# Kernel tuning notes

Measured on AMD Instinct MI355X. Metric: run time of the kernel, lower is better.

The kernel has to match this reference:

```python
import jax, jax.numpy as jnp
import numpy as np
import math

B = 2048; H = 16; KL = 16; KR = 16; D = 64
K_MAX = 32; MAX_DEPTH = 12; DE = 32; DEPTH = 3


def setup_inputs() -> dict:
    key = jax.random.key(0)
    ks = jax.random.split(key, 8)
    def n(k, shape, s=1.0):
        return jax.random.normal(k, shape, dtype=jnp.float32) * s
    return {
        'f_left': n(ks[0], (B, H, KL, D)),
        'f_right': n(ks[1], (B, H, KR, D)),
        'gate_left_w': n(ks[2], (2 * D + DE, D), 0.02),
        'gate_left_b': jnp.full((D,), 0.5, jnp.float32),
        'gate_right_w': n(ks[3], (2 * D + DE, D), 0.02),
        'gate_right_b': jnp.full((D,), 0.5, jnp.float32),
        'parent_query_base': n(ks[4], (K_MAX, D), 0.02),
        'query_offset_w': n(ks[5], (DE, K_MAX * D), 0.02),
        'query_offset_b': jnp.zeros((K_MAX * D,), jnp.float32),
        'ln_gamma': jnp.ones((D,), jnp.float32),
        'ln_beta': jnp.zeros((D,), jnp.float32),
        'skip_proj_w': n(ks[6], (D, D), 0.02),
        'skip_alpha': jnp.float32(0.1),
        'wave_freq': jnp.linspace(0.3, 4.0, H, dtype=jnp.float32),
        'wave_damp': jnp.linspace(-3.0, 0.5, H, dtype=jnp.float32),
        'wave_phase': jnp.linspace(0.0, math.pi, H, dtype=jnp.float32),
        'depth': DEPTH,
    }


def _depth_vec(depth):
    # sinusoidal embedding row for `depth` (interleaved sin/cos)
    inv = jnp.exp(jnp.arange(0, DE, 2, dtype=jnp.float32) * (-math.log(10000.0) / DE))
    return jnp.stack([jnp.sin(depth * inv), jnp.cos(depth * inv)], axis=1).reshape(-1)


def _forward(f_left, f_right, glw, glb, grw, grb, pqb, qow, qob, g, b, spw, sa, wf, wd, wp, depth):
    # wave rotation of right child (complex multiply on split halves)
    scale = float(max(2 ** (MAX_DEPTH - depth), 1))
    alpha_d = jax.nn.softplus(wd) / scale
    omega_d = wf / scale
    phi_d = wp + depth * (math.pi / 4.0)
    decay = jnp.exp(-alpha_d * scale)
    pr = (decay * jnp.cos(omega_d * scale + phi_d))[None, :, None, None]  # (1,H,1,1)
    pi_ = (decay * jnp.sin(omega_d * scale + phi_d))[None, :, None, None]
    d2 = D // 2
    fr, fi = f_right[..., :d2], f_right[..., d2:]
    rot = jnp.concatenate([pr * fr - pi_ * fi, pi_ * fr + pr * fi], axis=-1)  # (B,H,KR,D)

    # depth-conditioned gating
    left_mean = f_left.mean(axis=2)   # (B,H,D)
    right_mean = rot.mean(axis=2)
    dv = _depth_vec(depth)            # (DE,)
    dvb = jnp.broadcast_to(dv, (f_left.shape[0], H, DE))
    gate_in = jnp.concatenate([left_mean, right_mean, dvb], axis=-1)  # (B,H,2D+DE)
    g_l = jax.nn.sigmoid(gate_in @ glw + glb)[:, :, None, :]
    g_r = jax.nn.sigmoid(gate_in @ grw + grb)[:, :, None, :]
    bank = jnp.concatenate([f_left * g_l, rot * g_r], axis=2)  # (B,H,KL+KR,D)

    # small-K attention with depth-offset parent queries
    k_parent = min(KL + KR, K_MAX)
    q_off = (dv @ qow + qob).reshape(K_MAX, D)
    pq = pqb[:k_parent] + q_off[:k_parent]  # (k_parent,D)
    attn = jax.nn.softmax(jnp.einsum('qd,bhkd->bhqk', pq, bank) / math.sqrt(D), axis=-1)
    parent_raw = jnp.einsum('bhqk,bhkd->bhqd', attn, bank)  # (B,H,k_parent,D)

    # layernorm over D (eps=1e-5, biased var as in torch)
    mu = parent_raw.mean(axis=-1, keepdims=True)
    var = parent_raw.var(axis=-1, keepdims=True)
    parent_norm = (parent_raw - mu) / jnp.sqrt(var + 1e-5) * g + b

    # gated skip from left mean
    skip = (left_mean @ spw)[:, :, None, :]
    return parent_norm + jax.nn.sigmoid(sa) * skip


def reference(f_left, f_right, gate_left_w, gate_left_b, gate_right_w, gate_right_b, parent_query_base, query_offset_w, query_offset_b, ln_gamma, ln_beta, skip_proj_w, skip_alpha, wave_freq, wave_damp, wave_phase, depth):
    return _forward(f_left, f_right, gate_left_w, gate_left_b, gate_right_w, gate_right_b, parent_query_base, query_offset_w, query_offset_b, ln_gamma, ln_beta, skip_proj_w, skip_alpha, wave_freq, wave_damp, wave_phase, depth)
```

## Files before the change

kernel.cpp:

```cpp
#include <hip/hip_runtime.h>
#include <math.h>

#define B_ 2048
#define H_ 16
#define D_ 64
#define DE_ 32
#define NK_ 32
#define KP_ 32

#define OFF_WTL 2048
#define OFF_WTR 10240
#define OFF_SPT 18432
#define OFF_BL  22528
#define WS_TOTAL 22656

typedef __attribute__((ext_vector_type(8)))  short short8;
typedef __attribute__((ext_vector_type(16))) float f32x16;
typedef __attribute__((ext_vector_type(4)))  unsigned int uint4v;

#define MFMA32(A,Bo,C) __builtin_amdgcn_mfma_f32_32x32x16_bf16(A,Bo,C,0,0,0)

__device__ __forceinline__ unsigned short bf16_rne(float x){
    unsigned u = __float_as_uint(x);
    unsigned r = u + 0x7fffu + ((u>>16)&1u);
    return (unsigned short)(r>>16);
}
__device__ __forceinline__ float bf16_to_f(unsigned short h){
    return __uint_as_float((unsigned)h << 16);
}
__device__ __forceinline__ unsigned pack2(unsigned short a, unsigned short b){
    return (unsigned)a | ((unsigned)b << 16);
}

__global__ void precompute(const float* __restrict__ pqb,
                           const float* __restrict__ qow,
                           const float* __restrict__ qob,
                           const float* __restrict__ glw,
                           const float* __restrict__ glb,
                           const float* __restrict__ grw,
                           const float* __restrict__ grb,
                           const float* __restrict__ spw,
                           const int*   __restrict__ depth_p,
                           float* __restrict__ ws)
{
    __shared__ float dvS[DE_];
    const int t = threadIdx.x;
    const int depth = depth_p[0];
    if (t < DE_) {
        int pi_ = t >> 1;
        float inv = expf(-(float)(2*pi_) * (logf(10000.f)/(float)DE_));
        float x = (float)depth * inv;
        dvS[t] = (t & 1) ? cosf(x) : sinf(x);
    }
    __syncthreads();
    int idx = blockIdx.x*256 + t;
    if (idx < 2048) {
        int q = idx >> 6, d = idx & 63;
        float acc = pqb[idx] + qob[idx];
        for (int i = 0; i < DE_; ++i) acc += dvS[i]*qow[i*2048 + idx];
        unsigned short hi = bf16_rne(acc);
        unsigned short lo = bf16_rne(acc - bf16_to_f(hi));
        int ds = d >> 4, h2 = (d>>3)&1, jj = d&7;
        int e = (ds*64 + (h2*32 + q))*8 + jj;
        unsigned short* wsu = (unsigned short*)ws;
        wsu[e]        = hi;
        wsu[2048 + e] = lo;
    } else if (idx < 2048 + 8192) {
        int j = idx - 2048; int d = j >> 7, i = j & 127;
        ws[OFF_WTL + j] = glw[i*64 + d];
    } else if (idx < 2048 + 16384) {
        int j = idx - (2048+8192); int d = j >> 7, i = j & 127;
        ws[OFF_WTR + j] = grw[i*64 + d];
    } else if (idx < 2048 + 16384 + 4096) {
        int j = idx - (2048+16384); int d = j >> 6, i = j & 63;
        ws[OFF_SPT + j] = spw[i*64 + d];
    } else if (idx < WS_TOTAL) {
        int j = idx - OFF_BL; int side = j >> 6, d = j & 63;
        const float* W = side ? grw : glw;
        float acc = side ? grb[d] : glb[d];
        for (int i = 0; i < DE_; ++i) acc += dvS[i]*W[(128+i)*64 + d];
        ws[OFF_BL + j] = acc;
    }
}

__global__ __launch_bounds__(256, 4)
void gwm_main(const float* __restrict__ fL, const float* __restrict__ fR,
              const float* __restrict__ lng, const float* __restrict__ lnb,
              const float* __restrict__ sa,
              const float* __restrict__ wf, const float* __restrict__ wd,
              const float* __restrict__ wp, const int* __restrict__ depth_p,
              const float* __restrict__ ws, float* __restrict__ out)
{
    __shared__ __align__(16) unsigned short bankH16[NK_*64];
    __shared__ __align__(16) unsigned short bankL16[NK_*64];
    __shared__ __align__(16) unsigned short bTH16[64*40];
    __shared__ __align__(16) unsigned short bTL16[64*40];
    __shared__ __align__(16) float partialS[8][64];
    __shared__ __align__(16) float lrS[128];
    __shared__ __align__(16) float glS[64], grS[64], addS[64], gamS[64];

    const int t    = threadIdx.x;
    const int pair = blockIdx.x;
    const int h    = pair & (H_-1);
    const int wv   = t >> 6;
    const int lane = t & 63;
    const int depth = depth_p[0];

    float wdv = wd[h];
    float sp = logf(1.f + expf(wdv));
    float decay = expf(-sp);
    float ang = wf[h] + wp[h] + (float)depth * 0.78539816339744831f;
    float pr  = decay * cosf(ang);
    float pim = decay * sinf(ang);

    const int kk = t >> 4;
    const int c  = t & 15;

    const size_t base = (size_t)pair * (16*64);
    float4 v4 = *(const float4*)(fL + base + kk*64 + 4*c);
    const float* fp = fR + base + kk*64;
    float2 fr2 = *(const float2*)(fp + 2*c);
    float2 fi2 = *(const float2*)(fp + 2*c + 32);
    float ro0 = pr*fr2.x - pim*fi2.x;
    float ro1 = pr*fr2.y - pim*fi2.y;
    float ro2 = pim*fr2.x + pr*fi2.x;
    float ro3 = pim*fr2.y + pr*fi2.y;

    float s0=v4.x, s1=v4.y, s2=v4.z, s3=v4.w;
    float u0=ro0, u1=ro1, u2=ro2, u3=ro3;
#define RED2(x) { x += __shfl_xor(x,16); x += __shfl_xor(x,32); }
    RED2(s0) RED2(s1) RED2(s2) RED2(s3)
    RED2(u0) RED2(u1) RED2(u2) RED2(u3)
    if (lane < 16) {
        *(float4*)(&partialS[wv][4*c])      = make_float4(s0,s1,s2,s3);
        *(float2*)(&partialS[4+wv][2*c])    = make_float2(u0,u1);
        *(float2*)(&partialS[4+wv][2*c+32]) = make_float2(u2,u3);
    }
    __syncthreads();

    if (t < 128) {
        int d = t & 63, side = t >> 6;
        const float* p = &partialS[side*4][0];
        lrS[t] = (p[d] + p[64+d] + p[128+d] + p[192+d]) * 0.0625f;
    }
    __syncthreads();

    if (wv < 2) {
        const float* Wt = ws + (wv ? OFF_WTR : OFF_WTL) + lane*128;
        float acc = ws[OFF_BL + wv*64 + lane];
        #pragma unroll 8
        for (int i = 0; i < 128; i += 4) {
            float4 w = *(const float4*)(Wt + i);
            float4 v = *(const float4*)(lrS + i);
            acc += w.x*v.x + w.y*v.y + w.z*v.z + w.w*v.w;
        }
        float g = 1.f / (1.f + __expf(-acc));
        (wv ? grS : glS)[lane] = g;
    } else if (wv == 2) {
        const float* Sp = ws + OFF_SPT + lane*64;
        float acc = 0.f;
        #pragma unroll 8
        for (int i = 0; i < 64; i += 4) {
            float4 w = *(const float4*)(Sp + i);
            float4 v = *(const float4*)(lrS + i);
            acc += w.x*v.x + w.y*v.y + w.z*v.z + w.w*v.w;
        }
        float ss = 1.f / (1.f + __expf(-sa[0]));
        addS[lane] = lnb[lane] + ss * acc;
    } else {
        gamS[lane] = lng[lane];
    }
    __syncthreads();

    const int hw = pair & 3;
    short8 qh0, qh1, qh2, qh3, ql0, ql1, ql2, ql3;
    if (wv == hw) {
        const unsigned short* wsu = (const unsigned short*)ws;
        qh0 = *(const short8*)(wsu + (0*64 + lane)*8);
        qh1 = *(const short8*)(wsu + (1*64 + lane)*8);
        qh2 = *(const short8*)(wsu + (2*64 + lane)*8);
        qh3 = *(const short8*)(wsu + (3*64 + lane)*8);
        ql0 = *(const short8*)(wsu + 2048 + (0*64 + lane)*8);
        ql1 = *(const short8*)(wsu + 2048 + (1*64 + lane)*8);
        ql2 = *(const short8*)(wsu + 2048 + (2*64 + lane)*8);
        ql3 = *(const short8*)(wsu + 2048 + (3*64 + lane)*8);
    }

    {
        float4 g4 = *(const float4*)(glS + 4*c);
        float b0 = v4.x*g4.x, b1 = v4.y*g4.y, b2 = v4.z*g4.z, b3 = v4.w*g4.w;
        unsigned short H0=bf16_rne(b0), H1=bf16_rne(b1), H2=bf16_rne(b2), H3=bf16_rne(b3);
        unsigned short L0=bf16_rne(b0-bf16_to_f(H0)), L1=bf16_rne(b1-bf16_to_f(H1));
        unsigned short L2=bf16_rne(b2-bf16_to_f(H2)), L3=bf16_rne(b3-bf16_to_f(H3));
        const int m = (kk & 7) << 3;
        int eo = kk*64 + ((4*c) ^ m);
        *(uint2*)(bankH16 + eo) = make_uint2(pack2(H0,H1), pack2(H2,H3));
        *(uint2*)(bankL16 + eo) = make_uint2(pack2(L0,L1), pack2(L2,L3));
        bTH16[(4*c+0)*40 + kk] = H0; bTH16[(4*c+1)*40 + kk] = H1;
        bTH16[(4*c+2)*40 + kk] = H2; bTH16[(4*c+3)*40 + kk] = H3;
        bTL16[(4*c+0)*40 + kk] = L0; bTL16[(4*c+1)*40 + kk] = L1;
        bTL16[(4*c+2)*40 + kk] = L2; bTL16[(4*c+3)*40 + kk] = L3;

        float2 ga = *(const float2*)(grS + 2*c);
        float2 gb = *(const float2*)(grS + 2*c + 32);
        float w0 = ro0*ga.x, w1 = ro1*ga.y, w2 = ro2*gb.x, w3 = ro3*gb.y;
        unsigned short R0=bf16_rne(w0), R1=bf16_rne(w1), R2=bf16_rne(w2), R3=bf16_rne(w3);
        unsigned short S0_=bf16_rne(w0-bf16_to_f(R0)), S1_=bf16_rne(w1-bf16_to_f(R1));
        unsigned short S2_=bf16_rne(w2-bf16_to_f(R2)), S3_=bf16_rne(w3-bf16_to_f(R3));
        const int row = (16+kk)*64;
        *(unsigned*)(bankH16 + row + ((2*c)    ^ m)) = pack2(R0,R1);
        *(unsigned*)(bankH16 + row + ((2*c+32) ^ m)) = pack2(R2,R3);
        *(unsigned*)(bankL16 + row + ((2*c)    ^ m)) = pack2(S0_,S1_);
        *(unsigned*)(bankL16 + row + ((2*c+32) ^ m)) = pack2(S2_,S3_);
        bTH16[(2*c  )*40 + 16+kk] = R0; bTH16[(2*c+1 )*40 + 16+kk] = R1;
        bTH16[(2*c+32)*40 + 16+kk] = R2; bTH16[(2*c+33)*40 + 16+kk] = R3;
        bTL16[(2*c  )*40 + 16+kk] = S0_; bTL16[(2*c+1 )*40 + 16+kk] = S1_;
        bTL16[(2*c+32)*40 + 16+kk] = S2_; bTL16[(2*c+33)*40 + 16+kk] = S3_;
    }
    __syncthreads();

    if (wv == hw) {
        const int q  = lane & 31;
        const int hh = lane >> 5;

        f32x16 A1, A2;
        #pragma unroll
        for (int i = 0; i < 16; ++i) { A1[i] = 0.f; A2[i] = 0.f; }
        const int sw = (q & 7) << 3;
        {
            int eo = q*64 + ((0*16 + hh*8) ^ sw);
            short8 ah = *(const short8*)(bankH16 + eo);
            short8 al = *(const short8*)(bankL16 + eo);
            A1 = MFMA32(ah, qh0, A1); A2 = MFMA32(ah, ql0, A2); A1 = MFMA32(al, qh0, A1);
        }
        {
            int eo = q*64 + ((1*16 + hh*8) ^ sw);
            short8 ah = *(const short8*)(bankH16 + eo);
            short8 al = *(const short8*)(bankL16 + eo);
            A1 = MFMA32(ah, qh1, A1); A2 = MFMA32(ah, ql1, A2); A1 = MFMA32(al, qh1, A1);
        }
        {
            int eo = q*64 + ((2*16 + hh*8) ^ sw);
            short8 ah = *(const short8*)(bankH16 + eo);
            short8 al = *(const short8*)(bankL16 + eo);
            A1 = MFMA32(ah, qh2, A1); A2 = MFMA32(ah, ql2, A2); A1 = MFMA32(al, qh2, A1);
        }
        {
            int eo = q*64 + ((3*16 + hh*8) ^ sw);
            short8 ah = *(const short8*)(bankH16 + eo);
            short8 al = *(const short8*)(bankL16 + eo);
            A1 = MFMA32(ah, qh3, A1); A2 = MFMA32(ah, ql3, A2); A1 = MFMA32(al, qh3, A1);
        }
        float sc[16];
        #pragma unroll
        for (int i = 0; i < 16; ++i) sc[i] = (A1[i] + A2[i]) * 0.125f;
        float mx = sc[0];
        #pragma unroll
        for (int i = 1; i < 16; ++i) mx = fmaxf(mx, sc[i]);
        mx = fmaxf(mx, __shfl_xor(mx, 32));
        float ssum = 0.f;
        #pragma unroll
        for (int i = 0; i < 16; ++i) { sc[i] = __expf(sc[i] - mx); ssum += sc[i]; }
        ssum += __shfl_xor(ssum, 32);
        float inv = 1.f / ssum;
        unsigned ch[8], cl[8], dh[8], dl[8];
        #pragma unroll
        for (int w = 0; w < 8; ++w) {
            float a0 = sc[2*w]*inv, a1 = sc[2*w+1]*inv;
            unsigned short Ha = bf16_rne(a0), Hb = bf16_rne(a1);
            unsigned short La = bf16_rne(a0 - bf16_to_f(Ha));
            unsigned short Lb = bf16_rne(a1 - bf16_to_f(Hb));
            ch[w] = pack2(Ha,Hb); cl[w] = pack2(La,Lb);
        }
        #pragma unroll
        for (int w = 0; w < 8; ++w) { dh[w] = __shfl_xor(ch[w],32); dl[w] = __shfl_xor(cl[w],32); }
        short8 Bh0, Bh1, Bl0, Bl1;
        if (hh == 0) {
            uint4v vh0 = {ch[0],ch[1],dh[0],dh[1]}, vl0 = {cl[0],cl[1],dl[0],dl[1]};
            uint4v vh1 = {ch[4],ch[5],dh[4],dh[5]}, vl1 = {cl[4],cl[5],dl[4],dl[5]};
            Bh0 = __builtin_bit_cast(short8, vh0); Bl0 = __builtin_bit_cast(short8, vl0);
            Bh1 = __builtin_bit_cast(short8, vh1); Bl1 = __builtin_bit_cast(short8, vl1);
        } else {
            uint4v vh0 = {dh[2],dh[3],ch[2],ch[3]}, vl0 = {dl[2],dl[3],cl[2],cl[3]};
            uint4v vh1 = {dh[6],dh[7],ch[6],ch[7]}, vl1 = {dl[6],dl[7],cl[6],cl[7]};
            Bh0 = __builtin_bit_cast(short8, vh0); Bl0 = __builtin_bit_cast(short8, vl0);
            Bh1 = __builtin_bit_cast(short8, vh1); Bl1 = __builtin_bit_cast(short8, vl1);
        }
        f32x16 P0, P1;
        {
            f32x16 p1, p2;
            #pragma unroll
            for (int i = 0; i < 16; ++i) { p1[i] = 0.f; p2[i] = 0.f; }
            int e0 = q*40 + hh*8;
            short8 Ah = *(const short8*)(bTH16 + e0);
            short8 Al = *(const short8*)(bTL16 + e0);
            p1 = MFMA32(Ah, Bh0, p1); p2 = MFMA32(Ah, Bl0, p2); p1 = MFMA32(Al, Bh0, p1);
            int e1 = q*40 + 16 + hh*8;
            Ah = *(const short8*)(bTH16 + e1);
            Al = *(const short8*)(bTL16 + e1);
            p1 = MFMA32(Ah, Bh1, p1); p2 = MFMA32(Ah, Bl1, p2); p1 = MFMA32(Al, Bh1, p1);
            P0 = p1 + p2;
        }
        {
            f32x16 p1, p2;
            #pragma unroll
            for (int i = 0; i < 16; ++i) { p1[i] = 0.f; p2[i] = 0.f; }
            int e0 = (32+q)*40 + hh*8;
            short8 Ah = *(const short8*)(bTH16 + e0);
            short8 Al = *(const short8*)(bTL16 + e0);
            p1 = MFMA32(Ah, Bh0, p1); p2 = MFMA32(Ah, Bl0, p2); p1 = MFMA32(Al, Bh0, p1);
            int e1 = (32+q)*40 + 16 + hh*8;
            Ah = *(const short8*)(bTH16 + e1);
            Al = *(const short8*)(bTL16 + e1);
            p1 = MFMA32(Ah, Bh1, p1); p2 = MFMA32(Ah, Bl1, p2); p1 = MFMA32(Al, Bh1, p1);
            P1 = p1 + p2;
        }
        float sum = 0.f;
        #pragma unroll
        for (int i = 0; i < 16; ++i) sum += P0[i] + P1[i];
        sum += __shfl_xor(sum, 32);
        float mu = sum * (1.f/64.f);
        float ssd = 0.f;
        #pragma unroll
        for (int i = 0; i < 16; ++i) {
            float d1 = P0[i]-mu, d2 = P1[i]-mu;
            ssd += d1*d1 + d2*d2;
        }
        ssd += __shfl_xor(ssd, 32);
        float rinv = 1.f / sqrtf(ssd*(1.f/64.f) + 1e-5f);
        float* outp = out + (size_t)pair*(KP_*D_) + (size_t)q*64;
        #pragma unroll
        for (int grp = 0; grp < 4; ++grp) {
            int d0 = grp*8 + hh*4;
            float4 gm = *(const float4*)(gamS + d0);
            float4 ad = *(const float4*)(addS + d0);
            float4 o;
            o.x = (P0[grp*4+0]-mu)*rinv*gm.x + ad.x;
            o.y = (P0[grp*4+1]-mu)*rinv*gm.y + ad.y;
            o.z = (P0[grp*4+2]-mu)*rinv*gm.z + ad.z;
            o.w = (P0[grp*4+3]-mu)*rinv*gm.w + ad.w;
            *(float4*)(outp + d0) = o;
            int d1 = 32 + d0;
            float4 gm1 = *(const float4*)(gamS + d1);
            float4 ad1 = *(const float4*)(addS + d1);
            float4 o1;
            o1.x = (P1[grp*4+0]-mu)*rinv*gm1.x + ad1.x;
            o1.y = (P1[grp*4+1]-mu)*rinv*gm1.y + ad1.y;
            o1.z = (P1[grp*4+2]-mu)*rinv*gm1.z + ad1.z;
            o1.w = (P1[grp*4+3]-mu)*rinv*gm1.w + ad1.w;
            *(float4*)(outp + d1) = o1;
        }
    }
}

extern "C" void kernel_launch(void* const* d_in, const int* in_sizes, int n_in,
                              void* d_out, int out_size, void* d_ws, size_t ws_size,
                              hipStream_t stream) {
    const float* fL  = (const float*)d_in[0];
    const float* fR  = (const float*)d_in[1];
    const float* glw = (const float*)d_in[2];
    const float* glb = (const float*)d_in[3];
    const float* grw = (const float*)d_in[4];
    const float* grb = (const float*)d_in[5];
    const float* pqb = (const float*)d_in[6];
    const float* qow = (const float*)d_in[7];
    const float* qob = (const float*)d_in[8];
    const float* lng = (const float*)d_in[9];
    const float* lnb = (const float*)d_in[10];
    const float* spw = (const float*)d_in[11];
    const float* sa  = (const float*)d_in[12];
    const float* wf  = (const float*)d_in[13];
    const float* wd  = (const float*)d_in[14];
    const float* wp  = (const float*)d_in[15];
    const int* depth = (const int*)d_in[16];
    float* ws  = (float*)d_ws;
    float* out = (float*)d_out;

    hipLaunchKernelGGL(precompute, dim3((WS_TOTAL+255)/256), dim3(256), 0, stream,
                       pqb, qow, qob, glw, glb, grw, grb, spw, depth, ws);
    hipLaunchKernelGGL(gwm_main, dim3(B_*H_), dim3(256), 0, stream,
                       fL, fR, lng, lnb, sa, wf, wd, wp, depth, ws, out);
}
```

Baseline: 712.3 us.

## Read gate weights in original layout with coalesced float4 loads; split MFMA accumulators

The precompute kernel no longer builds transposed copies of the gate and skip weights. The main kernel now reads them directly in row-major order: each 16-lane group handles one input row and four output columns with float4 loads, and shuffles reduce across the groups. This makes the per-block weight reads coalesced instead of strided per lane and shrinks the precompute work. Separately, the error-compensation MFMA chains now use independent accumulators, which shortens the dependent MFMA latency chains at the cost of extra registers.

```diff
diff --git a/kernel.cpp b/kernel.cpp
--- a/kernel.cpp
+++ b/kernel.cpp
@@ -8,11 +8,8 @@
 #define NK_ 32
 #define KP_ 32
 
-#define OFF_WTL 2048
-#define OFF_WTR 10240
-#define OFF_SPT 18432
-#define OFF_BL  22528
-#define WS_TOTAL 22656
+#define OFF_BL   2048
+#define WS_TOTAL 2176
 
 typedef __attribute__((ext_vector_type(8)))  short short8;
 typedef __attribute__((ext_vector_type(16))) float f32x16;
@@ -39,7 +36,6 @@
                            const float* __restrict__ glb,
                            const float* __restrict__ grw,
                            const float* __restrict__ grb,
-                           const float* __restrict__ spw,
                            const int*   __restrict__ depth_p,
                            float* __restrict__ ws)
 {
@@ -65,15 +61,6 @@
         unsigned short* wsu = (unsigned short*)ws;
         wsu[e]        = hi;
         wsu[2048 + e] = lo;
-    } else if (idx < 2048 + 8192) {
-        int j = idx - 2048; int d = j >> 7, i = j & 127;
-        ws[OFF_WTL + j] = glw[i*64 + d];
-    } else if (idx < 2048 + 16384) {
-        int j = idx - (2048+8192); int d = j >> 7, i = j & 127;
-        ws[OFF_WTR + j] = grw[i*64 + d];
-    } else if (idx < 2048 + 16384 + 4096) {
-        int j = idx - (2048+16384); int d = j >> 6, i = j & 63;
-        ws[OFF_SPT + j] = spw[i*64 + d];
     } else if (idx < WS_TOTAL) {
         int j = idx - OFF_BL; int side = j >> 6, d = j & 63;
         const float* W = side ? grw : glw;
@@ -85,6 +72,8 @@
 
 __global__ __launch_bounds__(256, 4)
 void gwm_main(const float* __restrict__ fL, const float* __restrict__ fR,
+              const float* __restrict__ glw, const float* __restrict__ grw,
+              const float* __restrict__ spw,
               const float* __restrict__ lng, const float* __restrict__ lnb,
               const float* __restrict__ sa,
               const float* __restrict__ wf, const float* __restrict__ wd,
@@ -145,30 +134,54 @@
     }
     __syncthreads();
 
-    if (wv < 2) {
-        const float* Wt = ws + (wv ? OFF_WTR : OFF_WTL) + lane*128;
-        float acc = ws[OFF_BL + wv*64 + lane];
-        #pragma unroll 8
-        for (int i = 0; i < 128; i += 4) {
-            float4 w = *(const float4*)(Wt + i);
-            float4 v = *(const float4*)(lrS + i);
-            acc += w.x*v.x + w.y*v.y + w.z*v.z + w.w*v.w;
-        }
-        float g = 1.f / (1.f + __expf(-acc));
-        (wv ? grS : glS)[lane] = g;
-    } else if (wv == 2) {
-        const float* Sp = ws + OFF_SPT + lane*64;
-        float acc = 0.f;
-        #pragma unroll 8
-        for (int i = 0; i < 64; i += 4) {
-            float4 w = *(const float4*)(Sp + i);
-            float4 v = *(const float4*)(lrS + i);
-            acc += w.x*v.x + w.y*v.y + w.z*v.z + w.w*v.w;
-        }
-        float ss = 1.f / (1.f + __expf(-sa[0]));
-        addS[lane] = lnb[lane] + ss * acc;
-    } else {
-        gamS[lane] = lng[lane];
+    {
+        const int g  = lane >> 4;
+        const int c4 = (lane & 15) * 4;
+        if (wv < 2) {
+            const float* W = wv ? grw : glw;
+            float4 bb = *(const float4*)(ws + OFF_BL + wv*64 + c4);
+            float a0=0.f, a1=0.f, a2=0.f, a3=0.f;
+            #pragma unroll 8
+            for (int i0 = 0; i0 < 128; i0 += 4) {
+                float4 w = *(const float4*)(W + (size_t)(i0+g)*64 + c4);
+                float x = lrS[i0+g];
+                a0 += x*w.x; a1 += x*w.y; a2 += x*w.z; a3 += x*w.w;
+            }
+            a0 += __shfl_xor(a0,16); a1 += __shfl_xor(a1,16);
+            a2 += __shfl_xor(a2,16); a3 += __shfl_xor(a3,16);
+            a0 += __shfl_xor(a0,32); a1 += __shfl_xor(a1,32);
+            a2 += __shfl_xor(a2,32); a3 += __shfl_xor(a3,32);
+            if (lane < 16) {
+                float4 gg;
+                gg.x = 1.f/(1.f + __expf(-(a0 + bb.x)));
+                gg.y = 1.f/(1.f + __expf(-(a1 + bb.y)));
+                gg.z = 1.f/(1.f + __expf(-(a2 + bb.z)));
+                gg.w = 1.f/(1.f + __expf(-(a3 + bb.w)));
+                *(float4*)((wv ? grS : glS) + c4) = gg;
+            }
+        } else if (wv == 2) {
+            float4 lb = *(const float4*)(lnb + c4);
+            float sigsa = 1.f / (1.f + __expf(-sa[0]));
+            float a0=0.f, a1=0.f, a2=0.f, a3=0.f;
+            #pragma unroll 8
+            for (int i0 = 0; i0 < 64; i0 += 4) {
+                float4 w = *(const float4*)(spw + (size_t)(i0+g)*64 + c4);
+                float x = lrS[i0+g];
+                a0 += x*w.x; a1 += x*w.y; a2 += x*w.z; a3 += x*w.w;
+            }
+            a0 += __shfl_xor(a0,16); a1 += __shfl_xor(a1,16);
+            a2 += __shfl_xor(a2,16); a3 += __shfl_xor(a3,16);
+            a0 += __shfl_xor(a0,32); a1 += __shfl_xor(a1,32);
+            a2 += __shfl_xor(a2,32); a3 += __shfl_xor(a3,32);
+            if (lane < 16) {
+                float4 av;
+                av.x = lb.x + sigsa*a0; av.y = lb.y + sigsa*a1;
+                av.z = lb.z + sigsa*a2; av.w = lb.w + sigsa*a3;
+                *(float4*)(addS + c4) = av;
+            }
+        } else {
+            gamS[lane] = lng[lane];
+        }
     }
     __syncthreads();
 
@@ -223,37 +236,37 @@
         const int q  = lane & 31;
         const int hh = lane >> 5;
 
-        f32x16 A1, A2;
-        #pragma unroll
-        for (int i = 0; i < 16; ++i) { A1[i] = 0.f; A2[i] = 0.f; }
+        f32x16 A1, A2, A3;
+        #pragma unroll
+        for (int i = 0; i < 16; ++i) { A1[i] = 0.f; A2[i] = 0.f; A3[i] = 0.f; }
         const int sw = (q & 7) << 3;
         {
             int eo = q*64 + ((0*16 + hh*8) ^ sw);
             short8 ah = *(const short8*)(bankH16 + eo);
             short8 al = *(const short8*)(bankL16 + eo);
-            A1 = MFMA32(ah, qh0, A1); A2 = MFMA32(ah, ql0, A2); A1 = MFMA32(al, qh0, A1);
+            A1 = MFMA32(ah, qh0, A1); A2 = MFMA32(ah, ql0, A2); A3 = MFMA32(al, qh0, A3);
         }
         {
             int eo = q*64 + ((1*16 + hh*8) ^ sw);
             short8 ah = *(const short8*)(bankH16 + eo);
             short8 al = *(const short8*)(bankL16 + eo);
-            A1 = MFMA32(ah, qh1, A1); A2 = MFMA32(ah, ql1, A2); A1 = MFMA32(al, qh1, A1);
+            A1 = MFMA32(ah, qh1, A1); A2 = MFMA32(ah, ql1, A2); A3 = MFMA32(al, qh1, A3);
         }
         {
             int eo = q*64 + ((2*16 + hh*8) ^ sw);
             short8 ah = *(const short8*)(bankH16 + eo);
             short8 al = *(const short8*)(bankL16 + eo);
-            A1 = MFMA32(ah, qh2, A1); A2 = MFMA32(ah, ql2, A2); A1 = MFMA32(al, qh2, A1);
+            A1 = MFMA32(ah, qh2, A1); A2 = MFMA32(ah, ql2, A2); A3 = MFMA32(al, qh2, A3);
         }
         {
             int eo = q*64 + ((3*16 + hh*8) ^ sw);
             short8 ah = *(const short8*)(bankH16 + eo);
             short8 al = *(const short8*)(bankL16 + eo);
-            A1 = MFMA32(ah, qh3, A1); A2 = MFMA32(ah, ql3, A2); A1 = MFMA32(al, qh3, A1);
+            A1 = MFMA32(ah, qh3, A1); A2 = MFMA32(ah, ql3, A2); A3 = MFMA32(al, qh3, A3);
         }
         float sc[16];
         #pragma unroll
-        for (int i = 0; i < 16; ++i) sc[i] = (A1[i] + A2[i]) * 0.125f;
+        for (int i = 0; i < 16; ++i) sc[i] = (A1[i] + A2[i] + A3[i]) * 0.125f;
         float mx = sc[0];
         #pragma unroll
         for (int i = 1; i < 16; ++i) mx = fmaxf(mx, sc[i]);
@@ -298,7 +311,7 @@
             int e1 = q*40 + 16 + hh*8;
             Ah = *(const short8*)(bTH16 + e1);
             Al = *(const short8*)(bTL16 + e1);
-            p1 = MFMA32(Ah, Bh1, p1); p2 = MFMA32(Ah, Bl1, p2); p1 = MFMA32(Al, Bh1, p1);
+            p1 = MFMA32(Ah, Bh1, p1); p2 = MFMA32(Ah, Bl1, p2); p2 = MFMA32(Al, Bh1, p2);
             P0 = p1 + p2;
         }
         {
@@ -312,7 +325,7 @@
             int e1 = (32+q)*40 + 16 + hh*8;
             Ah = *(const short8*)(bTH16 + e1);
             Al = *(const short8*)(bTL16 + e1);
-            p1 = MFMA32(Ah, Bh1, p1); p2 = MFMA32(Ah, Bl1, p2); p1 = MFMA32(Al, Bh1, p1);
+            p1 = MFMA32(Ah, Bh1, p1); p2 = MFMA32(Ah, Bl1, p2); p2 = MFMA32(Al, Bh1, p2);
             P1 = p1 + p2;
         }
         float sum = 0.f;
@@ -377,7 +390,7 @@
     float* out = (float*)d_out;
 
     hipLaunchKernelGGL(precompute, dim3((WS_TOTAL+255)/256), dim3(256), 0, stream,
-                       pqb, qow, qob, glw, glb, grw, grb, spw, depth, ws);
+                       pqb, qow, qob, glw, glb, grw, grb, depth, ws);
     hipLaunchKernelGGL(gwm_main, dim3(B_*H_), dim3(256), 0, stream,
-                       fL, fR, lng, lnb, sa, wf, wd, wp, depth, ws, out);
-}
+                       fL, fR, glw, grw, spw, lng, lnb, sa, wf, wd, wp, depth, ws, out);
+}
```

New measurement: 589.3 us. 17.3% less time.
